# Performance work log

Measured on AMD Instinct MI355X. Metric: run time of the kernel, lower is better.

Reference implementation:

```python
import jax, jax.numpy as jnp
import numpy as np

NLAYER = 4


def setup_inputs() -> dict:
    key = jax.random.key(0)
    k1, k2, k3 = jax.random.split(key, 3)
    B, T, D, H, L = 32, 512, 512, 512, NLAYER
    scale = 1.0 / np.sqrt(H)
    inputs = jax.random.normal(k1, (B, T, D), dtype=jnp.float32)
    W = jax.random.normal(k2, (L, 3, H, H), dtype=jnp.float32) * scale
    U = jax.random.normal(k3, (L, 3, D, H), dtype=jnp.float32) * scale
    return {"inputs": inputs, "W": W, "U": U}


def _gru_stack(inputs, W, U):
    # inputs: [B, T, D]; W: [L, 3, H, H]; U: [L, 3, D, H]
    L = W.shape[0]
    H = W.shape[-1]
    B = inputs.shape[0]
    x_tbd = jnp.transpose(inputs, (1, 0, 2))  # [T, B, D]
    init = jnp.zeros((L, B, H), dtype=inputs.dtype)

    def step(prev, xt):
        inp = xt
        new_states = []
        for i in range(L):
            z = jax.nn.sigmoid(inp @ U[i, 0] + prev[i] @ W[i, 0])
            r = jax.nn.sigmoid(inp @ U[i, 1] + prev[i] @ W[i, 1])
            h = jnp.tanh(inp @ U[i, 2] + (r * prev[i]) @ W[i, 2])
            s = (1.0 - z) * h + z * prev[i]
            inp = s
            new_states.append(s)
        new = jnp.stack(new_states)  # [L, B, H]
        return new, new_states[-1]  # emit top-layer state

    _, ys = jax.lax.scan(step, init, x_tbd)  # ys: [T, B, H]
    return jnp.transpose(ys, (1, 0, 2))  # [B, T, H]


def reference(inputs, W, U):
    return _gru_stack(inputs, W, U)
```

## Files before the change

### kernel.cpp

```cpp
#include <hip/hip_runtime.h>

#define BB 32
#define TT 512
#define DD 512
#define HH 512
#define LL 4
#define HB (HH * BB)
#define NWG 192
#define TPB 256

#define STATE_FLOATS (LL * 2 * HB)
#define GATE_FLOATS  (3 * LL * HB)
#define DATA_FLOATS  (STATE_FLOATS + GATE_FLOATS)
#define FLAG_STRIDE  64
#define NFLAG        209
#define FLAGS_BYTES  ((unsigned long long)NFLAG * FLAG_STRIDE * 4ull)
#define WS_NEED_BYTES ((unsigned long long)DATA_FLOATS * 4ull + FLAGS_BYTES)

#define KC    64
#define NCH   (HH / KC)
#define IBR   68
#define IBF   (BB * IBR)
#define WLDS  32768
#define LDS_BYTES ((WLDS + 2 * IBF) * 4)

#define DONE_A(f, i) ((f) + (i) * FLAG_STRIDE)
#define DONE_B(f, i) ((f) + (8 + (i)) * FLAG_STRIDE)
#define SPIN_CAP (1 << 22)

__device__ __forceinline__ void wg_wait(int* cnt, int target, int& dead) {
    if (threadIdx.x == 0 && !dead) {
        int spins = 0;
        while (__hip_atomic_load(cnt, __ATOMIC_RELAXED,
                                 __HIP_MEMORY_SCOPE_AGENT) < target) {
            __builtin_amdgcn_s_sleep(2);
            if (++spins > SPIN_CAP) { dead = 1; break; }
        }
        (void)__hip_atomic_load(cnt, __ATOMIC_ACQUIRE,
                                __HIP_MEMORY_SCOPE_AGENT);
    }
    __syncthreads();
}

__device__ __forceinline__ void wg_post(int* cnt) {
    asm volatile("" ::: "memory");
    __builtin_amdgcn_s_waitcnt(0);
    __syncthreads();
    if (threadIdx.x == 0)
        atomicAdd(cnt, 1);
}

__device__ __forceinline__ void pub_store(float* p, float v) {
    __hip_atomic_store(p, v, __ATOMIC_RELAXED, __HIP_MEMORY_SCOPE_AGENT);
}
__device__ __forceinline__ float sigf(float v) {
    return 1.0f / (1.0f + __expf(-v));
}

#define FMA16(WV, E0, E1, E2, E3)                                           \
    acc[0][0] = fmaf(E0, WV.x, acc[0][0]); acc[0][1] = fmaf(E0, WV.y, acc[0][1]); \
    acc[0][2] = fmaf(E0, WV.z, acc[0][2]); acc[0][3] = fmaf(E0, WV.w, acc[0][3]); \
    acc[1][0] = fmaf(E1, WV.x, acc[1][0]); acc[1][1] = fmaf(E1, WV.y, acc[1][1]); \
    acc[1][2] = fmaf(E1, WV.z, acc[1][2]); acc[1][3] = fmaf(E1, WV.w, acc[1][3]); \
    acc[2][0] = fmaf(E2, WV.x, acc[2][0]); acc[2][1] = fmaf(E2, WV.y, acc[2][1]); \
    acc[2][2] = fmaf(E2, WV.z, acc[2][2]); acc[2][3] = fmaf(E2, WV.w, acc[2][3]); \
    acc[3][0] = fmaf(E3, WV.x, acc[3][0]); acc[3][1] = fmaf(E3, WV.y, acc[3][1]); \
    acc[3][2] = fmaf(E3, WV.z, acc[3][2]); acc[3][3] = fmaf(E3, WV.w, acc[3][3])


__global__ __launch_bounds__(TPB) void gru_wave(
    const float* __restrict__ x,
    const float* __restrict__ Wp,
    const float* __restrict__ Up,
    float* __restrict__ out,
    float* __restrict__ ws)
{
    extern __shared__ float lds[];

    const int bid = blockIdx.x;
    const int wg  = (bid & 7) * 24 + (bid >> 3);
    const int tid = threadIdx.x;
    const int sb  = tid >> 4;
    const int sk  = tid & 15;

    float* state = ws;
    float* zbuf  = state + LL * 2 * HB;
    float* rbuf  = zbuf + LL * HB;
    float* hUbuf = rbuf + LL * HB;
    int*   flags = (int*)(ws + DATA_FLOATS);

    float* ib0 = lds + WLDS;
    float* ib1 = ib0 + IBF;

    const bool isZR = wg < 128;
    const bool isHU = (wg >= 128) && (wg < 160);

    int iA = 0, gA = 0, col0 = 0, iB = 0, col0B = 0;
    if (isZR) { int grp = wg >> 4; iA = grp >> 1; gA = grp & 1; col0 = (wg & 15) * 32; }
    else if (isHU) { int w2 = wg - 128; iA = w2 >> 3; col0 = (w2 & 7) * 64; }
    else { int w3 = wg - 160; iB = w3 >> 3; col0B = (w3 & 7) * 64; }

    if (isZR) {
        const float* Um = Up + (size_t)(iA * 3 + gA) * DD * HH + col0;
        const float* Wm = Wp + (size_t)(iA * 3 + gA) * HH * HH + col0;
        for (int u = tid; u < 4096; u += TPB) {
            int k = u >> 3, cc = u & 7;
            *(float4*)&lds[u * 4]         = *(const float4*)&Um[(size_t)k * HH + cc * 4];
            *(float4*)&lds[16384 + u * 4] = *(const float4*)&Wm[(size_t)k * HH + cc * 4];
        }
    } else {
        const float* Mm = isHU ? (Up + (size_t)(iA * 3 + 2) * DD * HH + col0)
                               : (Wp + (size_t)(iB * 3 + 2) * HH * HH + col0B);
        for (int u = tid; u < 8192; u += TPB) {
            int k = u >> 4, cc = u & 15;
            *(float4*)&lds[u * 4] = *(const float4*)&Mm[(size_t)k * HH + cc * 4];
        }
    }
    __syncthreads();

    int dead = 0;

    if (isZR) {
        const int ksc = tid & 3, cq = (tid >> 2) & 7, bq = tid >> 5;
        const int colq = col0 + cq * 4;
        float* dst = (gA == 0 ? zbuf : rbuf) + (size_t)iA * HB;
        int* cb_up = (iA > 0) ? DONE_B(flags, iA - 1) : nullptr;
        int* cb_my = DONE_B(flags, iA);
        int* c_my  = DONE_A(flags, iA);
        for (int t = 0; t < TT; ++t) {
            float acc[4][4] = {};
            if (cb_up) wg_wait(cb_up, 8 * (t + 1), dead);
            {
                const float* src; size_t rstr;
                if (iA == 0) {
                    src = x + (size_t)sb * TT * DD + (size_t)t * DD + sk * 4;
                    rstr = (size_t)16 * TT * DD;
                } else {
                    src = state + (size_t)((iA - 1) * 2 + (t & 1)) * HB + sb * HH + sk * 4;
                    rstr = (size_t)16 * HH;
                }
                float4 g0 = *(const float4*)&src[0];
                float4 g1 = *(const float4*)&src[rstr];
                src += KC;
                *(float4*)&ib0[sb * IBR + sk * 4]        = g0;
                *(float4*)&ib0[(sb + 16) * IBR + sk * 4] = g1;
                g0 = *(const float4*)&src[0]; g1 = *(const float4*)&src[rstr]; src += KC;
                __syncthreads();
                float *rb = ib0, *nb = ib1;
                const float* wp0 = lds + (ksc * 16 * 8 + cq) * 4;
                for (int c = 0; c < NCH; ++c) {
                    const float* r0 = rb + (bq * 4 + 0) * IBR + ksc * 16;
                    const float* r1 = rb + (bq * 4 + 1) * IBR + ksc * 16;
                    const float* r2 = rb + (bq * 4 + 2) * IBR + ksc * 16;
                    const float* r3 = rb + (bq * 4 + 3) * IBR + ksc * 16;
                    const float* wp = wp0 + c * (KC * 8 * 4);
                    #pragma unroll
                    for (int kk = 0; kk < 4; ++kk) {
                        float4 x0 = *(const float4*)&r0[kk * 4];
                        float4 x1 = *(const float4*)&r1[kk * 4];
                        float4 x2 = *(const float4*)&r2[kk * 4];
                        float4 x3 = *(const float4*)&r3[kk * 4];
                        #pragma unroll
                        for (int j = 0; j < 4; ++j) {
                            float4 wv = *(const float4*)&wp[(kk * 4 + j) * 32];
                            FMA16(wv, (&x0.x)[j], (&x1.x)[j], (&x2.x)[j], (&x3.x)[j]);
                        }
                    }
                    if (c < NCH - 1) {
                        *(float4*)&nb[sb * IBR + sk * 4]        = g0;
                        *(float4*)&nb[(sb + 16) * IBR + sk * 4] = g1;
                        if (c < NCH - 2) {
                            g0 = *(const float4*)&src[0];
                            g1 = *(const float4*)&src[rstr];
                            src += KC;
                        }
                    }
                    __syncthreads();
                    float* tp = rb; rb = nb; nb = tp;
                }
            }
            wg_wait(cb_my, 8 * t, dead);
            {
                const float* src = state + (size_t)(iA * 2 + ((t + 1) & 1)) * HB
                                 + sb * HH + sk * 4;
                const size_t rstr = (size_t)16 * HH;
                float4 g0 = *(const float4*)&src[0];
                float4 g1 = *(const float4*)&src[rstr];
                src += KC;
                *(float4*)&ib0[sb * IBR + sk * 4]        = g0;
                *(float4*)&ib0[(sb + 16) * IBR + sk * 4] = g1;
                g0 = *(const float4*)&src[0]; g1 = *(const float4*)&src[rstr]; src += KC;
                __syncthreads();
                float *rb = ib0, *nb = ib1;
                const float* wp0 = lds + 16384 + (ksc * 16 * 8 + cq) * 4;
                for (int c = 0; c < NCH; ++c) {
                    const float* r0 = rb + (bq * 4 + 0) * IBR + ksc * 16;
                    const float* r1 = rb + (bq * 4 + 1) * IBR + ksc * 16;
                    const float* r2 = rb + (bq * 4 + 2) * IBR + ksc * 16;
                    const float* r3 = rb + (bq * 4 + 3) * IBR + ksc * 16;
                    const float* wp = wp0 + c * (KC * 8 * 4);
                    #pragma unroll
                    for (int kk = 0; kk < 4; ++kk) {
                        float4 x0 = *(const float4*)&r0[kk * 4];
                        float4 x1 = *(const float4*)&r1[kk * 4];
                        float4 x2 = *(const float4*)&r2[kk * 4];
                        float4 x3 = *(const float4*)&r3[kk * 4];
                        #pragma unroll
                        for (int j = 0; j < 4; ++j) {
                            float4 wv = *(const float4*)&wp[(kk * 4 + j) * 32];
                            FMA16(wv, (&x0.x)[j], (&x1.x)[j], (&x2.x)[j], (&x3.x)[j]);
                        }
                    }
                    if (c < NCH - 1) {
                        *(float4*)&nb[sb * IBR + sk * 4]        = g0;
                        *(float4*)&nb[(sb + 16) * IBR + sk * 4] = g1;
                        if (c < NCH - 2) {
                            g0 = *(const float4*)&src[0];
                            g1 = *(const float4*)&src[rstr];
                            src += KC;
                        }
                    }
                    __syncthreads();
                    float* tp = rb; rb = nb; nb = tp;
                }
            }
            #pragma unroll
            for (int i = 0; i < 4; ++i)
                #pragma unroll
                for (int j = 0; j < 4; ++j) {
                    float v = acc[i][j];
                    v += __shfl_xor(v, 1, 64);
                    v += __shfl_xor(v, 2, 64);
                    acc[i][j] = v;
                }
            float s0, s1, s2, s3;
            if      (ksc == 0) { s0 = acc[0][0]; s1 = acc[0][1]; s2 = acc[0][2]; s3 = acc[0][3]; }
            else if (ksc == 1) { s0 = acc[1][0]; s1 = acc[1][1]; s2 = acc[1][2]; s3 = acc[1][3]; }
            else if (ksc == 2) { s0 = acc[2][0]; s1 = acc[2][1]; s2 = acc[2][2]; s3 = acc[2][3]; }
            else               { s0 = acc[3][0]; s1 = acc[3][1]; s2 = acc[3][2]; s3 = acc[3][3]; }
            float* drow = dst + (size_t)(bq * 4 + ksc) * HH + colq;
            pub_store(&drow[0], sigf(s0));
            pub_store(&drow[1], sigf(s1));
            pub_store(&drow[2], sigf(s2));
            pub_store(&drow[3], sigf(s3));
            wg_post(c_my);
        }
    } else if (isHU) {
        const int ks2 = tid & 1, cq = (tid >> 1) & 15, bq = tid >> 5;
        const int colq = col0 + cq * 4;
        float* hu = hUbuf + (size_t)iA * HB;
        int* cb_up = (iA > 0) ? DONE_B(flags, iA - 1) : nullptr;
        int* cb_my = DONE_B(flags, iA);
        int* c_my  = DONE_A(flags, iA);
        for (int t = 0; t < TT; ++t) {
            float acc[4][4] = {};
            if (cb_up) wg_wait(cb_up, 8 * (t + 1), dead);
            {
                const float* src; size_t rstr;
                if (iA == 0) {
                    src = x + (size_t)sb * TT * DD + (size_t)t * DD + sk * 4;
                    rstr = (size_t)16 * TT * DD;
                } else {
                    src = state + (size_t)((iA - 1) * 2 + (t & 1)) * HB + sb * HH + sk * 4;
                    rstr = (size_t)16 * HH;
                }
                float4 g0 = *(const float4*)&src[0];
                float4 g1 = *(const float4*)&src[rstr];
                src += KC;
                *(float4*)&ib0[sb * IBR + sk * 4]        = g0;
                *(float4*)&ib0[(sb + 16) * IBR + sk * 4] = g1;
                g0 = *(const float4*)&src[0]; g1 = *(const float4*)&src[rstr]; src += KC;
                __syncthreads();
                float *rb = ib0, *nb = ib1;
                const float* wp0 = lds + (ks2 * 32 * 16 + cq) * 4;
                for (int c = 0; c < NCH; ++c) {
                    const float* r0 = rb + (bq * 4 + 0) * IBR + ks2 * 32;
                    const float* r1 = rb + (bq * 4 + 1) * IBR + ks2 * 32;
                    const float* r2 = rb + (bq * 4 + 2) * IBR + ks2 * 32;
                    const float* r3 = rb + (bq * 4 + 3) * IBR + ks2 * 32;
                    const float* wp = wp0 + c * (KC * 16 * 4);
                    #pragma unroll
                    for (int kk = 0; kk < 8; ++kk) {
                        float4 x0 = *(const float4*)&r0[kk * 4];
                        float4 x1 = *(const float4*)&r1[kk * 4];
                        float4 x2 = *(const float4*)&r2[kk * 4];
                        float4 x3 = *(const float4*)&r3[kk * 4];
                        #pragma unroll
                        for (int j = 0; j < 4; ++j) {
                            float4 wv = *(const float4*)&wp[(kk * 4 + j) * 64];
                            FMA16(wv, (&x0.x)[j], (&x1.x)[j], (&x2.x)[j], (&x3.x)[j]);
                        }
                    }
                    if (c < NCH - 1) {
                        *(float4*)&nb[sb * IBR + sk * 4]        = g0;
                        *(float4*)&nb[(sb + 16) * IBR + sk * 4] = g1;
                        if (c < NCH - 2) {
                            g0 = *(const float4*)&src[0];
                            g1 = *(const float4*)&src[rstr];
                            src += KC;
                        }
                    }
                    __syncthreads();
                    float* tp = rb; rb = nb; nb = tp;
                }
            }
            wg_wait(cb_my, 8 * t, dead);
            #pragma unroll
            for (int i = 0; i < 4; ++i)
                #pragma unroll
                for (int j = 0; j < 4; ++j) {
                    float v = acc[i][j];
                    v += __shfl_xor(v, 1, 64);
                    acc[i][j] = v;
                }
            float r0v[4], r1v[4];
            if (ks2 == 0) {
                r0v[0]=acc[0][0]; r0v[1]=acc[0][1]; r0v[2]=acc[0][2]; r0v[3]=acc[0][3];
                r1v[0]=acc[1][0]; r1v[1]=acc[1][1]; r1v[2]=acc[1][2]; r1v[3]=acc[1][3];
            } else {
                r0v[0]=acc[2][0]; r0v[1]=acc[2][1]; r0v[2]=acc[2][2]; r0v[3]=acc[2][3];
                r1v[0]=acc[3][0]; r1v[1]=acc[3][1]; r1v[2]=acc[3][2]; r1v[3]=acc[3][3];
            }
            const int b0 = bq * 4 + ks2 * 2;
            float* h0 = hu + (size_t)b0 * HH + colq;
            float* h1 = hu + (size_t)(b0 + 1) * HH + colq;
            pub_store(&h0[0], r0v[0]); pub_store(&h0[1], r0v[1]);
            pub_store(&h0[2], r0v[2]); pub_store(&h0[3], r0v[3]);
            pub_store(&h1[0], r1v[0]); pub_store(&h1[1], r1v[1]);
            pub_store(&h1[2], r1v[2]); pub_store(&h1[3], r1v[3]);
            wg_post(c_my);
        }
    } else {
        const int ks2 = tid & 1, cq = (tid >> 1) & 15, bq = tid >> 5;
        const int colq = col0B + cq * 4;
        const float* rbase = rbuf + (size_t)iB * HB;
        const float* hu    = hUbuf + (size_t)iB * HB;
        const float* zz    = zbuf + (size_t)iB * HB;
        int* c_my = DONE_B(flags, iB);
        for (int t = 0; t < TT; ++t) {
            wg_wait(DONE_A(flags, iB), 40 * (t + 1), dead);
            const float* prow = state + (size_t)(iB * 2 + ((t + 1) & 1)) * HB;
            float acc[4][4] = {};
            {
                const float* rs = rbase + (size_t)sb * HH + sk * 4;
                const float* ps = prow  + (size_t)sb * HH + sk * 4;
                const size_t rstr = (size_t)16 * HH;
                float4 g0r = *(const float4*)&rs[0],   g0p = *(const float4*)&ps[0];
                float4 g1r = *(const float4*)&rs[rstr], g1p = *(const float4*)&ps[rstr];
                rs += KC; ps += KC;
                *(float4*)&ib0[sb * IBR + sk * 4] =
                    make_float4(g0r.x * g0p.x, g0r.y * g0p.y, g0r.z * g0p.z, g0r.w * g0p.w);
                *(float4*)&ib0[(sb + 16) * IBR + sk * 4] =
                    make_float4(g1r.x * g1p.x, g1r.y * g1p.y, g1r.z * g1p.z, g1r.w * g1p.w);
                g0r = *(const float4*)&rs[0];   g0p = *(const float4*)&ps[0];
                g1r = *(const float4*)&rs[rstr]; g1p = *(const float4*)&ps[rstr];
                rs += KC; ps += KC;
                __syncthreads();
                float *rb = ib0, *nb = ib1;
                const float* wp0 = lds + (ks2 * 32 * 16 + cq) * 4;
                for (int c = 0; c < NCH; ++c) {
                    const float* r0 = rb + (bq * 4 + 0) * IBR + ks2 * 32;
                    const float* r1 = rb + (bq * 4 + 1) * IBR + ks2 * 32;
                    const float* r2 = rb + (bq * 4 + 2) * IBR + ks2 * 32;
                    const float* r3 = rb + (bq * 4 + 3) * IBR + ks2 * 32;
                    const float* wp = wp0 + c * (KC * 16 * 4);
                    #pragma unroll
                    for (int kk = 0; kk < 8; ++kk) {
                        float4 x0 = *(const float4*)&r0[kk * 4];
                        float4 x1 = *(const float4*)&r1[kk * 4];
                        float4 x2 = *(const float4*)&r2[kk * 4];
                        float4 x3 = *(const float4*)&r3[kk * 4];
                        #pragma unroll
                        for (int j = 0; j < 4; ++j) {
                            float4 wv = *(const float4*)&wp[(kk * 4 + j) * 64];
                            FMA16(wv, (&x0.x)[j], (&x1.x)[j], (&x2.x)[j], (&x3.x)[j]);
                        }
                    }
                    if (c < NCH - 1) {
                        *(float4*)&nb[sb * IBR + sk * 4] =
                            make_float4(g0r.x * g0p.x, g0r.y * g0p.y, g0r.z * g0p.z, g0r.w * g0p.w);
                        *(float4*)&nb[(sb + 16) * IBR + sk * 4] =
                            make_float4(g1r.x * g1p.x, g1r.y * g1p.y, g1r.z * g1p.z, g1r.w * g1p.w);
                        if (c < NCH - 2) {
                            g0r = *(const float4*)&rs[0];   g0p = *(const float4*)&ps[0];
                            g1r = *(const float4*)&rs[rstr]; g1p = *(const float4*)&ps[rstr];
                            rs += KC; ps += KC;
                        }
                    }
                    __syncthreads();
                    float* tp = rb; rb = nb; nb = tp;
                }
            }
            if (iB < 3) wg_wait(DONE_A(flags, iB + 1), 40 * t, dead);
            #pragma unroll
            for (int i = 0; i < 4; ++i)
                #pragma unroll
                for (int j = 0; j < 4; ++j) {
                    float v = acc[i][j];
                    v += __shfl_xor(v, 1, 64);
                    acc[i][j] = v;
                }
            float r0v[4], r1v[4];
            if (ks2 == 0) {
                r0v[0]=acc[0][0]; r0v[1]=acc[0][1]; r0v[2]=acc[0][2]; r0v[3]=acc[0][3];
                r1v[0]=acc[1][0]; r1v[1]=acc[1][1]; r1v[2]=acc[1][2]; r1v[3]=acc[1][3];
            } else {
                r0v[0]=acc[2][0]; r0v[1]=acc[2][1]; r0v[2]=acc[2][2]; r0v[3]=acc[2][3];
                r1v[0]=acc[3][0]; r1v[1]=acc[3][1]; r1v[2]=acc[3][2]; r1v[3]=acc[3][3];
            }
            float* stNew = state + (size_t)(iB * 2 + (t & 1)) * HB;
            const int b0 = bq * 4 + ks2 * 2;
            #pragma unroll
            for (int ii = 0; ii < 2; ++ii) {
                const int b = b0 + ii;
                float4 hu4 = *(const float4*)&hu[(size_t)b * HH + colq];
                float4 zz4 = *(const float4*)&zz[(size_t)b * HH + colq];
                float4 pv4 = *(const float4*)&prow[(size_t)b * HH + colq];
                float* av = ii ? r1v : r0v;
                float4 o4;
                #pragma unroll
                for (int j = 0; j < 4; ++j) {
                    float h  = tanhf(av[j] + (&hu4.x)[j]);
                    float zg = (&zz4.x)[j];
                    float s  = zg * ((&pv4.x)[j] - h) + h;
                    pub_store(&stNew[(size_t)b * HH + colq + j], s);
                    (&o4.x)[j] = s;
                }
                if (iB == LL - 1)
                    *(float4*)&out[((size_t)b * TT + t) * HH + colq] = o4;
            }
            wg_post(c_my);
        }
    }
}

extern "C" void kernel_launch(void* const* d_in, const int* in_sizes, int n_in,
                              void* d_out, int out_size, void* d_ws, size_t ws_size,
                              hipStream_t stream) {
    const float* x  = (const float*)d_in[0];
    const float* Wp = (const float*)d_in[1];
    const float* Up = (const float*)d_in[2];
    float* out = (float*)d_out;
    float* ws  = (float*)d_ws;

    if (ws_size < WS_NEED_BYTES) {
        hipMemsetAsync(d_out, 0x7e, (size_t)out_size * sizeof(float), stream);
        return;
    }

    hipMemsetAsync(ws, 0, (size_t)STATE_FLOATS * sizeof(float), stream);
    hipMemsetAsync(ws + DATA_FLOATS, 0, FLAGS_BYTES, stream);

    hipLaunchKernelGGL(gru_wave, dim3(NWG), dim3(TPB), LDS_BYTES, stream,
                       x, Wp, Up, out, ws);
    hipError_t err = hipGetLastError();
    if (err != hipSuccess)
        hipMemsetAsync(d_out, 0x7f, (size_t)out_size * sizeof(float), stream);
}
```

Baseline: 14.08 ms.

## Split candidate-state stage across 16 workgroups per layer instead of 8

Raises the workgroup count from 192 to 224 so that each layer's W_h/state-update stage runs on 16 workgroups with 32 columns each, instead of 8 workgroups with 64 columns. The inner loop switches to a 4-way k split with a two-level shuffle reduction, and the completion-flag thresholds are doubled to match. This halves the per-workgroup work on the serial critical path of each timestep. In exchange it adds more workgroups to the spin-wait synchronization and puts more persistent blocks on the GPU.

```diff
diff --git a/kernel.cpp b/kernel.cpp
--- a/kernel.cpp
+++ b/kernel.cpp
@@ -6,7 +6,7 @@
 #define HH 512
 #define LL 4
 #define HB (HH * BB)
-#define NWG 192
+#define NWG 224
 #define TPB 256
 
 #define STATE_FLOATS (LL * 2 * HB)
@@ -78,7 +78,7 @@
     extern __shared__ float lds[];
 
     const int bid = blockIdx.x;
-    const int wg  = (bid & 7) * 24 + (bid >> 3);
+    const int wg  = (bid & 7) * 28 + (bid >> 3);
     const int tid = threadIdx.x;
     const int sb  = tid >> 4;
     const int sk  = tid & 15;
@@ -98,7 +98,7 @@
     int iA = 0, gA = 0, col0 = 0, iB = 0, col0B = 0;
     if (isZR) { int grp = wg >> 4; iA = grp >> 1; gA = grp & 1; col0 = (wg & 15) * 32; }
     else if (isHU) { int w2 = wg - 128; iA = w2 >> 3; col0 = (w2 & 7) * 64; }
-    else { int w3 = wg - 160; iB = w3 >> 3; col0B = (w3 & 7) * 64; }
+    else { int w3 = wg - 160; iB = w3 >> 4; col0B = (w3 & 15) * 32; }
 
     if (isZR) {
         const float* Um = Up + (size_t)(iA * 3 + gA) * DD * HH + col0;
@@ -108,11 +108,16 @@
             *(float4*)&lds[u * 4]         = *(const float4*)&Um[(size_t)k * HH + cc * 4];
             *(float4*)&lds[16384 + u * 4] = *(const float4*)&Wm[(size_t)k * HH + cc * 4];
         }
-    } else {
-        const float* Mm = isHU ? (Up + (size_t)(iA * 3 + 2) * DD * HH + col0)
-                               : (Wp + (size_t)(iB * 3 + 2) * HH * HH + col0B);
+    } else if (isHU) {
+        const float* Mm = Up + (size_t)(iA * 3 + 2) * DD * HH + col0;
         for (int u = tid; u < 8192; u += TPB) {
             int k = u >> 4, cc = u & 15;
+            *(float4*)&lds[u * 4] = *(const float4*)&Mm[(size_t)k * HH + cc * 4];
+        }
+    } else {
+        const float* Mm = Wp + (size_t)(iB * 3 + 2) * HH * HH + col0B;
+        for (int u = tid; u < 4096; u += TPB) {
+            int k = u >> 3, cc = u & 7;
             *(float4*)&lds[u * 4] = *(const float4*)&Mm[(size_t)k * HH + cc * 4];
         }
     }
@@ -129,7 +134,7 @@
         int* c_my  = DONE_A(flags, iA);
         for (int t = 0; t < TT; ++t) {
             float acc[4][4] = {};
-            if (cb_up) wg_wait(cb_up, 8 * (t + 1), dead);
+            if (cb_up) wg_wait(cb_up, 16 * (t + 1), dead);
             {
                 const float* src; size_t rstr;
                 if (iA == 0) {
@@ -179,7 +184,7 @@
                     float* tp = rb; rb = nb; nb = tp;
                 }
             }
-            wg_wait(cb_my, 8 * t, dead);
+            wg_wait(cb_my, 16 * t, dead);
             {
                 const float* src = state + (size_t)(iA * 2 + ((t + 1) & 1)) * HB
                                  + sb * HH + sk * 4;
@@ -254,7 +259,7 @@
         int* c_my  = DONE_A(flags, iA);
         for (int t = 0; t < TT; ++t) {
             float acc[4][4] = {};
-            if (cb_up) wg_wait(cb_up, 8 * (t + 1), dead);
+            if (cb_up) wg_wait(cb_up, 16 * (t + 1), dead);
             {
                 const float* src; size_t rstr;
                 if (iA == 0) {
@@ -304,7 +309,7 @@
                     float* tp = rb; rb = nb; nb = tp;
                 }
             }
-            wg_wait(cb_my, 8 * t, dead);
+            wg_wait(cb_my, 16 * t, dead);
             #pragma unroll
             for (int i = 0; i < 4; ++i)
                 #pragma unroll
@@ -331,7 +336,7 @@
             wg_post(c_my);
         }
     } else {
-        const int ks2 = tid & 1, cq = (tid >> 1) & 15, bq = tid >> 5;
+        const int ksc = tid & 3, cq = (tid >> 2) & 7, bq = tid >> 5;
         const int colq = col0B + cq * 4;
         const float* rbase = rbuf + (size_t)iB * HB;
         const float* hu    = hUbuf + (size_t)iB * HB;
@@ -357,22 +362,22 @@
                 rs += KC; ps += KC;
                 __syncthreads();
                 float *rb = ib0, *nb = ib1;
-                const float* wp0 = lds + (ks2 * 32 * 16 + cq) * 4;
+                const float* wp0 = lds + (ksc * 16 * 8 + cq) * 4;
                 for (int c = 0; c < NCH; ++c) {
-                    const float* r0 = rb + (bq * 4 + 0) * IBR + ks2 * 32;
-                    const float* r1 = rb + (bq * 4 + 1) * IBR + ks2 * 32;
-                    const float* r2 = rb + (bq * 4 + 2) * IBR + ks2 * 32;
-                    const float* r3 = rb + (bq * 4 + 3) * IBR + ks2 * 32;
-                    const float* wp = wp0 + c * (KC * 16 * 4);
+                    const float* r0 = rb + (bq * 4 + 0) * IBR + ksc * 16;
+                    const float* r1 = rb + (bq * 4 + 1) * IBR + ksc * 16;
+                    const float* r2 = rb + (bq * 4 + 2) * IBR + ksc * 16;
+                    const float* r3 = rb + (bq * 4 + 3) * IBR + ksc * 16;
+                    const float* wp = wp0 + c * (KC * 8 * 4);
                     #pragma unroll
-                    for (int kk = 0; kk < 8; ++kk) {
+                    for (int kk = 0; kk < 4; ++kk) {
                         float4 x0 = *(const float4*)&r0[kk * 4];
                         float4 x1 = *(const float4*)&r1[kk * 4];
                         float4 x2 = *(const float4*)&r2[kk * 4];
                         float4 x3 = *(const float4*)&r3[kk * 4];
                         #pragma unroll
                         for (int j = 0; j < 4; ++j) {
-                            float4 wv = *(const float4*)&wp[(kk * 4 + j) * 64];
+                            float4 wv = *(const float4*)&wp[(kk * 4 + j) * 32];
                             FMA16(wv, (&x0.x)[j], (&x1.x)[j], (&x2.x)[j], (&x3.x)[j]);
                         }
                     }
@@ -398,37 +403,31 @@
                 for (int j = 0; j < 4; ++j) {
                     float v = acc[i][j];
                     v += __shfl_xor(v, 1, 64);
+                    v += __shfl_xor(v, 2, 64);
                     acc[i][j] = v;
                 }
-            float r0v[4], r1v[4];
-            if (ks2 == 0) {
-                r0v[0]=acc[0][0]; r0v[1]=acc[0][1]; r0v[2]=acc[0][2]; r0v[3]=acc[0][3];
-                r1v[0]=acc[1][0]; r1v[1]=acc[1][1]; r1v[2]=acc[1][2]; r1v[3]=acc[1][3];
-            } else {
-                r0v[0]=acc[2][0]; r0v[1]=acc[2][1]; r0v[2]=acc[2][2]; r0v[3]=acc[2][3];
-                r1v[0]=acc[3][0]; r1v[1]=acc[3][1]; r1v[2]=acc[3][2]; r1v[3]=acc[3][3];
-            }
+            float s0, s1, s2, s3;
+            if      (ksc == 0) { s0 = acc[0][0]; s1 = acc[0][1]; s2 = acc[0][2]; s3 = acc[0][3]; }
+            else if (ksc == 1) { s0 = acc[1][0]; s1 = acc[1][1]; s2 = acc[1][2]; s3 = acc[1][3]; }
+            else if (ksc == 2) { s0 = acc[2][0]; s1 = acc[2][1]; s2 = acc[2][2]; s3 = acc[2][3]; }
+            else               { s0 = acc[3][0]; s1 = acc[3][1]; s2 = acc[3][2]; s3 = acc[3][3]; }
             float* stNew = state + (size_t)(iB * 2 + (t & 1)) * HB;
-            const int b0 = bq * 4 + ks2 * 2;
+            const int b = bq * 4 + ksc;
+            float4 hu4 = *(const float4*)&hu[(size_t)b * HH + colq];
+            float4 zz4 = *(const float4*)&zz[(size_t)b * HH + colq];
+            float4 pv4 = *(const float4*)&prow[(size_t)b * HH + colq];
+            float av[4] = {s0, s1, s2, s3};
+            float4 o4;
             #pragma unroll
-            for (int ii = 0; ii < 2; ++ii) {
-                const int b = b0 + ii;
-                float4 hu4 = *(const float4*)&hu[(size_t)b * HH + colq];
-                float4 zz4 = *(const float4*)&zz[(size_t)b * HH + colq];
-                float4 pv4 = *(const float4*)&prow[(size_t)b * HH + colq];
-                float* av = ii ? r1v : r0v;
-                float4 o4;
-                #pragma unroll
-                for (int j = 0; j < 4; ++j) {
-                    float h  = tanhf(av[j] + (&hu4.x)[j]);
-                    float zg = (&zz4.x)[j];
-                    float s  = zg * ((&pv4.x)[j] - h) + h;
-                    pub_store(&stNew[(size_t)b * HH + colq + j], s);
-                    (&o4.x)[j] = s;
-                }
-                if (iB == LL - 1)
-                    *(float4*)&out[((size_t)b * TT + t) * HH + colq] = o4;
-            }
+            for (int j = 0; j < 4; ++j) {
+                float h  = tanhf(av[j] + (&hu4.x)[j]);
+                float zg = (&zz4.x)[j];
+                float s  = zg * ((&pv4.x)[j] - h) + h;
+                pub_store(&stNew[(size_t)b * HH + colq + j], s);
+                (&o4.x)[j] = s;
+            }
+            if (iB == LL - 1)
+                *(float4*)&out[((size_t)b * TT + t) * HH + colq] = o4;
             wg_post(c_my);
         }
     }
```

Result: faster. 12.34 ms (-12.3%).
